# Performance work log

Measured on AMD Instinct MI355X. Metric: run time of the kernel, lower is better.

Reference implementation:

```python
import jax, jax.numpy as jnp
import numpy as np

N = 100000
E = 500000
MEM = 128
NODE = 128
TIME = 64
EDGE = 64
MEAN_DT = 0.0
STD_DT = 1.0
EPSILON = 0.1
GAMMA = 0.1
NUM_ITERS = 1


def setup_inputs() -> dict:
    key = jax.random.key(0)
    ks = jax.random.split(key, 20)

    def p(k, shape, fan_in):
        return jax.random.normal(k, shape, jnp.float32) * (1.0 / np.sqrt(fan_in))

    D_EDGE = EDGE + TIME  # TransformerConv edge_dim
    inp = {
        "x": jax.random.normal(ks[0], (N, MEM + NODE), jnp.float32),
        "last_update": jax.random.uniform(ks[1], (N,), jnp.float32) * 1000.0,
        "edge_index": jax.random.randint(ks[2], (2, E), 0, N),
        "t": jax.random.uniform(ks[3], (E,), jnp.float32) * 1000.0,
        "msg": jax.random.normal(ks[4], (E, EDGE), jnp.float32),
        # TimeEncoder: Linear(1, TIME) then cos
        "w_time": p(ks[5], (TIME,), 1),
        "b_time": jnp.zeros((TIME,), jnp.float32),
        # enc_x: Linear(MEM+NODE, MEM)
        "W_enc": p(ks[6], (MEM, MEM + NODE), MEM + NODE),
        "b_enc": jnp.zeros((MEM,), jnp.float32),
        # TransformerConv (heads=1, out=MEM, root_weight=False)
        "Wq": p(ks[7], (MEM, MEM), MEM),
        "bq": jnp.zeros((MEM,), jnp.float32),
        "Wk": p(ks[8], (MEM, MEM), MEM),
        "bk": jnp.zeros((MEM,), jnp.float32),
        "Wv": p(ks[9], (MEM, MEM), MEM),
        "bv": jnp.zeros((MEM,), jnp.float32),
        "We": p(ks[10], (MEM, D_EDGE), D_EDGE),  # lin_edge, bias=False
        # AntiSymmetricConv
        "W_anti": p(ks[11], (MEM, MEM), MEM),
        "b_anti": jnp.zeros((MEM,), jnp.float32),
    }
    return inp


def _forward(x, last_update, t, msg, w_time, b_time, W_enc, b_enc,
             Wq, bq, Wk, bk, Wv, bv, We, W_anti, b_anti, edge_index):
    src = edge_index[0]  # j (message source)
    dst = edge_index[1]  # i (aggregation target)

    # time encoding of relative times
    rel_t = jnp.abs(last_update[src] - t)
    rel_t = (rel_t - MEAN_DT) / STD_DT
    time_feat = jnp.cos(rel_t[:, None] * w_time[None, :] + b_time[None, :])  # [E, TIME]

    edge_attr = jnp.concatenate([msg, time_feat], axis=-1)  # [E, EDGE+TIME]
    e_proj = edge_attr @ We.T  # [E, MEM], lin_edge (no bias)

    h = x @ W_enc.T + b_enc  # [N, MEM]

    # antisymmetric weight
    A = W_anti - W_anti.T - GAMMA * jnp.eye(MEM, dtype=x.dtype)
    scale = 1.0 / np.sqrt(MEM)

    def phi(xc):
        # TransformerConv, heads=1, root_weight=False
        q = (xc @ Wq.T + bq)[dst]                 # [E, MEM]
        k = (xc @ Wk.T + bk)[src] + e_proj        # [E, MEM]
        v = (xc @ Wv.T + bv)[src] + e_proj        # [E, MEM]
        alpha = jnp.sum(q * k, axis=-1) * scale   # [E]
        # segment softmax over destination nodes
        amax = jax.ops.segment_max(alpha, dst, num_segments=N)
        amax = jnp.where(jnp.isfinite(amax), amax, 0.0)
        ex = jnp.exp(alpha - amax[dst])
        denom = jax.ops.segment_sum(ex, dst, num_segments=N) + 1e-16
        w = ex / denom[dst]
        return jax.ops.segment_sum(w[:, None] * v, dst, num_segments=N)  # [N, MEM]

    for _ in range(NUM_ITERS):
        g = phi(h)
        g = h @ A.T + g + b_anti
        g = jnp.tanh(g)
        h = h + EPSILON * g

    return jnp.tanh(h)


def reference(x, last_update, edge_index, t, msg, w_time, b_time, W_enc, b_enc,
              Wq, bq, Wk, bk, Wv, bv, We, W_anti, b_anti):
    return _forward(x, last_update, t, msg, w_time, b_time, W_enc, b_enc,
                    Wq, bq, Wk, bk, Wv, bv, We, W_anti, b_anti, edge_index)
```

## Files before the change

kernel.cpp:

```cpp
#include <hip/hip_runtime.h>
#include <hip/hip_bf16.h>
#include <math.h>

#define N_NODES 100000
#define N_EDGES 500000
#define MEM 128
#define IN_DIM 256
#define EDGEF 64
#define D_EDGE 128
#define EPSILON 0.1f
#define GAMMA 0.1f
#define SCALE 0.08838834764831845f

#define NPB 8
#define NT 32
#define XP 264
#define HP 136
#define ET 64
#define EA_LD 200

typedef __attribute__((ext_vector_type(8))) short bf16x8;
typedef __attribute__((ext_vector_type(4))) float f32x4;

__device__ __forceinline__ short f2bs(float f) {
    __hip_bfloat16 b = __float2bfloat16(f);
    return *(short*)&b;
}
__device__ __forceinline__ float bs2f(short s) {
    __hip_bfloat16 b = *(__hip_bfloat16*)&s;
    return __bfloat162float(b);
}
__device__ __forceinline__ float2 up2(unsigned int u) {
    float2 r;
    r.x = __uint_as_float(u << 16);
    r.y = __uint_as_float(u & 0xffff0000u);
    return r;
}
__device__ __forceinline__ unsigned int pk2(float lo, float hi) {
    return (unsigned int)(unsigned short)f2bs(lo)
         | ((unsigned int)(unsigned short)f2bs(hi) << 16);
}
__device__ __forceinline__ void atomic_pk_add_bf16(unsigned short* addr, unsigned int data) {
    asm volatile("global_atomic_pk_add_bf16 %0, %1, off"
                 :: "v"(addr), "v"(data) : "memory");
}

__global__ void k_prep(const float* __restrict__ W_anti, const float* __restrict__ We,
                       const float* __restrict__ W_enc,
                       const float* __restrict__ Wq, const float* __restrict__ Wk,
                       const float* __restrict__ Wv,
                       float* __restrict__ Abuf, unsigned short* __restrict__ Web,
                       unsigned short* __restrict__ WencH, unsigned short* __restrict__ WencL,
                       unsigned short* __restrict__ Wqb, unsigned short* __restrict__ Wkb,
                       unsigned short* __restrict__ Wvb) {
    int idx = blockIdx.x * blockDim.x + threadIdx.x;
    float w = W_enc[idx];
    short hi = f2bs(w);
    WencH[idx] = (unsigned short)hi;
    WencL[idx] = (unsigned short)f2bs(w - bs2f(hi));
    if (idx < 16384) {
        int m = idx >> 7, d = idx & 127;
        float a = W_anti[m * 128 + d] - W_anti[d * 128 + m];
        if (m == d) a -= GAMMA;
        Abuf[idx] = a;
        Web[idx] = (unsigned short)f2bs(We[idx]);
        Wqb[idx] = (unsigned short)f2bs(Wq[idx]);
        Wkb[idx] = (unsigned short)f2bs(Wk[idx]);
        Wvb[idx] = (unsigned short)f2bs(Wv[idx]);
    }
}

__global__ __launch_bounds__(256) void k_node_proj(
    const float* __restrict__ x,
    const float* __restrict__ b_enc, const float* __restrict__ bq,
    const float* __restrict__ bk, const float* __restrict__ bv,
    const unsigned short* __restrict__ WencH, const unsigned short* __restrict__ WencL,
    const unsigned short* __restrict__ Wqb, const unsigned short* __restrict__ Wkb,
    const unsigned short* __restrict__ Wvb,
    float* __restrict__ h, unsigned short* __restrict__ q,
    unsigned short* __restrict__ k, unsigned short* __restrict__ v)
{
    __shared__ short xhi[NT][XP];
    __shared__ short xlo[NT][XP];
    __shared__ short hb[NT][HP];
    const int tid = threadIdx.x;
    const int n0 = blockIdx.x * NT;

    {
        int r = tid >> 3, seg = tid & 7;
        const float4* xp = (const float4*)(x + (size_t)(n0 + r) * IN_DIM + seg * 32);
        unsigned int* dh = (unsigned int*)&xhi[r][seg * 32];
        unsigned int* dl = (unsigned int*)&xlo[r][seg * 32];
#pragma unroll
        for (int i = 0; i < 8; i++) {
            float4 a = xp[i];
            float fs[4] = {a.x, a.y, a.z, a.w};
            unsigned short h2[4], l2[4];
#pragma unroll
            for (int j = 0; j < 4; j++) {
                short hbit = f2bs(fs[j]);
                h2[j] = (unsigned short)hbit;
                l2[j] = (unsigned short)f2bs(fs[j] - bs2f(hbit));
            }
            dh[2 * i]     = h2[0] | ((unsigned int)h2[1] << 16);
            dh[2 * i + 1] = h2[2] | ((unsigned int)h2[3] << 16);
            dl[2 * i]     = l2[0] | ((unsigned int)l2[1] << 16);
            dl[2 * i + 1] = l2[2] | ((unsigned int)l2[3] << 16);
        }
    }
    __syncthreads();

    const int wave = tid >> 6, lane = tid & 63;
    const int quad = lane >> 4, l16 = lane & 15;
    const int mt = wave & 1;
    const int nh = wave >> 1;

    f32x4 acc[4];
#pragma unroll
    for (int i = 0; i < 4; i++) acc[i] = (f32x4){0.f, 0.f, 0.f, 0.f};
#pragma unroll
    for (int ko = 0; ko < 8; ko++) {
        bf16x8 ah = *(const bf16x8*)&xhi[mt * 16 + l16][ko * 32 + quad * 8];
        bf16x8 al = *(const bf16x8*)&xlo[mt * 16 + l16][ko * 32 + quad * 8];
#pragma unroll
        for (int i = 0; i < 4; i++) {
            size_t boff = (size_t)(nh * 64 + i * 16 + l16) * IN_DIM + ko * 32 + quad * 8;
            bf16x8 bh = *(const bf16x8*)(WencH + boff);
            bf16x8 bl = *(const bf16x8*)(WencL + boff);
            acc[i] = __builtin_amdgcn_mfma_f32_16x16x32_bf16(ah, bh, acc[i], 0, 0, 0);
            acc[i] = __builtin_amdgcn_mfma_f32_16x16x32_bf16(al, bh, acc[i], 0, 0, 0);
            acc[i] = __builtin_amdgcn_mfma_f32_16x16x32_bf16(ah, bl, acc[i], 0, 0, 0);
        }
    }
#pragma unroll
    for (int i = 0; i < 4; i++) {
        int col = nh * 64 + i * 16 + l16;
        float be = b_enc[col];
#pragma unroll
        for (int r = 0; r < 4; r++) {
            int row = mt * 16 + quad * 4 + r;
            float hv = acc[i][r] + be;
            h[(size_t)(n0 + row) * MEM + col] = hv;
            hb[row][col] = f2bs(hv);
        }
    }
    __syncthreads();

#define QKV(Wb, BIAS, OUT)                                                        \
    {                                                                             \
        f32x4 a2[4];                                                              \
        for (int i = 0; i < 4; i++) a2[i] = (f32x4){0.f, 0.f, 0.f, 0.f};          \
        for (int ko = 0; ko < 4; ko++) {                                          \
            bf16x8 a = *(const bf16x8*)&hb[mt * 16 + l16][ko * 32 + quad * 8];    \
            for (int i = 0; i < 4; i++) {                                         \
                size_t boff = (size_t)(nh * 64 + i * 16 + l16) * MEM              \
                            + ko * 32 + quad * 8;                                 \
                bf16x8 b = *(const bf16x8*)(Wb + boff);                           \
                a2[i] = __builtin_amdgcn_mfma_f32_16x16x32_bf16(a, b, a2[i], 0, 0, 0); \
            }                                                                     \
        }                                                                         \
        for (int i = 0; i < 4; i++) {                                             \
            int col = nh * 64 + i * 16 + l16;                                     \
            float bb = BIAS[col];                                                 \
            for (int r = 0; r < 4; r++) {                                         \
                int row = mt * 16 + quad * 4 + r;                                 \
                OUT[(size_t)(n0 + row) * MEM + col] =                             \
                    (unsigned short)f2bs(a2[i][r] + bb);                          \
            }                                                                     \
        }                                                                         \
    }
    QKV(Wqb, bq, q)
    QKV(Wkb, bk, k)
    QKV(Wvb, bv, v)
#undef QKV
}

__global__ __launch_bounds__(256, 6) void k_edge_all(
    const int* __restrict__ ei, const float* __restrict__ last_update,
    const float* __restrict__ t, const float* __restrict__ msg,
    const float* __restrict__ w_time, const float* __restrict__ b_time,
    const unsigned short* __restrict__ Web,
    const unsigned short* __restrict__ q, const unsigned short* __restrict__ k,
    const unsigned short* __restrict__ v,
    unsigned short* __restrict__ agg, float* __restrict__ denom)
{
    __shared__ short sE[ET][EA_LD];
    __shared__ int s_src[ET], s_dst[ET];
    __shared__ float s_rel[ET];

    const int tid = threadIdx.x;
    const size_t e0 = (size_t)blockIdx.x * ET;

    if (tid < ET) {
        size_t e = e0 + tid;
        if (e < N_EDGES) {
            int sn = ei[e];
            s_src[tid] = sn;
            s_dst[tid] = ei[N_EDGES + e];
            s_rel[tid] = fabsf(last_update[sn] - t[e]);
        } else {
            s_src[tid] = 0; s_dst[tid] = 0; s_rel[tid] = 0.f;
        }
    }
    __syncthreads();

    {
        int j = tid >> 2, seg = tid & 3, k0 = seg * 32;
        size_t e = e0 + j;
        bool valid = (e < N_EDGES);
        float vals[32];
        if (seg < 2) {
            if (valid) {
                const float4* mp = (const float4*)(msg + e * EDGEF + k0);
#pragma unroll
                for (int i = 0; i < 8; i++) {
                    float4 a = mp[i];
                    vals[4 * i] = a.x; vals[4 * i + 1] = a.y;
                    vals[4 * i + 2] = a.z; vals[4 * i + 3] = a.w;
                }
            } else {
#pragma unroll
                for (int i = 0; i < 32; i++) vals[i] = 0.f;
            }
        } else {
            int td = k0 - 64;
            float rel = s_rel[j];
            const float4* wtp = (const float4*)(w_time + td);
            const float4* btp = (const float4*)(b_time + td);
#pragma unroll
            for (int i = 0; i < 8; i++) {
                float4 wt = wtp[i];
                float4 bt = btp[i];
                vals[4 * i]     = valid ? __cosf(rel * wt.x + bt.x) : 0.f;
                vals[4 * i + 1] = valid ? __cosf(rel * wt.y + bt.y) : 0.f;
                vals[4 * i + 2] = valid ? __cosf(rel * wt.z + bt.z) : 0.f;
                vals[4 * i + 3] = valid ? __cosf(rel * wt.w + bt.w) : 0.f;
            }
        }
        unsigned int* dp = (unsigned int*)&sE[j][k0];
#pragma unroll
        for (int i = 0; i < 16; i++) {
            unsigned int lo = (unsigned short)f2bs(vals[2 * i]);
            unsigned int hi = (unsigned short)f2bs(vals[2 * i + 1]);
            dp[i] = lo | (hi << 16);
        }
    }
    __syncthreads();

    const int wave = tid >> 6, lane = tid & 63;
    const int quad = lane >> 4, l16 = lane & 15;

    f32x4 acc[8];
#pragma unroll
    for (int i = 0; i < 8; i++) acc[i] = (f32x4){0.f, 0.f, 0.f, 0.f};
#pragma unroll
    for (int ko = 0; ko < 4; ko++) {
        bf16x8 a = *(const bf16x8*)&sE[wave * 16 + l16][ko * 32 + quad * 8];
#pragma unroll
        for (int i = 0; i < 8; i++) {
            bf16x8 b = *(const bf16x8*)(Web + (size_t)(i * 16 + l16) * D_EDGE + ko * 32 + quad * 8);
            acc[i] = __builtin_amdgcn_mfma_f32_16x16x32_bf16(a, b, acc[i], 0, 0, 0);
        }
    }
    __syncthreads();
#pragma unroll
    for (int i = 0; i < 8; i++)
#pragma unroll
        for (int r = 0; r < 4; r++)
            sE[wave * 16 + quad * 4 + r][i * 16 + l16] = f2bs(acc[i][r]);
    __syncthreads();

    const int base = wave * 16;
    const int d2 = lane * 2;
    if (e0 + base < N_EDGES) {
        for (int jj = 0; jj < 16; jj += 2) {
            int ja = base + jj, jb = ja + 1;
            int sa = s_src[ja], da = s_dst[ja];
            int sb = s_src[jb], db = s_dst[jb];
            float2 epa = up2(*(const unsigned int*)&sE[ja][d2]);
            float2 epb = up2(*(const unsigned int*)&sE[jb][d2]);
            float2 qa = up2(*(const unsigned int*)(q + (size_t)da * MEM + d2));
            float2 qb2 = up2(*(const unsigned int*)(q + (size_t)db * MEM + d2));
            float2 ka = up2(*(const unsigned int*)(k + (size_t)sa * MEM + d2));
            float2 kb2 = up2(*(const unsigned int*)(k + (size_t)sb * MEM + d2));
            float pa = qa.x * (ka.x + epa.x) + qa.y * (ka.y + epa.y);
            float pb = qb2.x * (kb2.x + epb.x) + qb2.y * (kb2.y + epb.y);
#pragma unroll
            for (int off = 1; off < 64; off <<= 1) {
                pa += __shfl_xor(pa, off, 64);
                pb += __shfl_xor(pb, off, 64);
            }
            float exa = __expf(pa * SCALE);
            float exb = __expf(pb * SCALE);
            float2 va = up2(*(const unsigned int*)(v + (size_t)sa * MEM + d2));
            float2 vb = up2(*(const unsigned int*)(v + (size_t)sb * MEM + d2));
            unsigned int pka = pk2(exa * (va.x + epa.x), exa * (va.y + epa.y));
            unsigned int pkb = pk2(exb * (vb.x + epb.x), exb * (vb.y + epb.y));
            atomic_pk_add_bf16(agg + (size_t)da * MEM + d2, pka);
            atomic_pk_add_bf16(agg + (size_t)db * MEM + d2, pkb);
            if (lane == 0) {
                unsafeAtomicAdd(&denom[da], exa);
                unsafeAtomicAdd(&denom[db], exb);
            }
        }
    }
}

__global__ __launch_bounds__(128) void k_final(
    const float* __restrict__ h, const unsigned short* __restrict__ agg,
    const float* __restrict__ denom, const float* __restrict__ Abuf,
    const float* __restrict__ b_anti, float* __restrict__ out)
{
    __shared__ float hsh[NPB][MEM];
    const int m = threadIdx.x;
    const int n0 = blockIdx.x * NPB;
    for (int j = 0; j < NPB; j++) hsh[j][m] = h[(size_t)(n0 + j) * MEM + m];
    __syncthreads();
    float acc[NPB];
    float ba = b_anti[m];
    for (int j = 0; j < NPB; j++) {
        float dn = denom[n0 + j] + 1e-16f;
        float ag = bs2f((short)agg[(size_t)(n0 + j) * MEM + m]);
        acc[j] = ba + ag / dn;
    }
    const float4* A4 = (const float4*)(Abuf + (size_t)m * MEM);
    for (int d4 = 0; d4 < MEM / 4; d4++) {
        float4 w = A4[d4];
        int d = d4 * 4;
        for (int j = 0; j < NPB; j++)
            acc[j] += w.x * hsh[j][d] + w.y * hsh[j][d + 1] + w.z * hsh[j][d + 2] + w.w * hsh[j][d + 3];
    }
    for (int j = 0; j < NPB; j++) {
        float hv = hsh[j][m] + EPSILON * tanhf(acc[j]);
        out[(size_t)(n0 + j) * MEM + m] = tanhf(hv);
    }
}

extern "C" void kernel_launch(void* const* d_in, const int* in_sizes, int n_in,
                              void* d_out, int out_size, void* d_ws, size_t ws_size,
                              hipStream_t stream) {
    const float* x          = (const float*)d_in[0];
    const float* last_update= (const float*)d_in[1];
    const int*   ei         = (const int*)  d_in[2];
    const float* t          = (const float*)d_in[3];
    const float* msg        = (const float*)d_in[4];
    const float* w_time     = (const float*)d_in[5];
    const float* b_time     = (const float*)d_in[6];
    const float* W_enc      = (const float*)d_in[7];
    const float* b_enc      = (const float*)d_in[8];
    const float* Wq         = (const float*)d_in[9];
    const float* bq         = (const float*)d_in[10];
    const float* Wk         = (const float*)d_in[11];
    const float* bk         = (const float*)d_in[12];
    const float* Wv         = (const float*)d_in[13];
    const float* bv         = (const float*)d_in[14];
    const float* We         = (const float*)d_in[15];
    const float* W_anti     = (const float*)d_in[16];
    const float* b_anti     = (const float*)d_in[17];
    float* out = (float*)d_out;

    float* ws = (float*)d_ws;
    size_t nm = (size_t)N_NODES * MEM;
    float* h     = ws;
    float* Abuf  = h + nm;
    unsigned short* agg = (unsigned short*)(Abuf + MEM * MEM);
    float* denom = (float*)(agg + nm);
    unsigned short* qb    = (unsigned short*)(denom + N_NODES);
    unsigned short* kb    = qb + nm;
    unsigned short* vb    = kb + nm;
    unsigned short* Web   = vb + nm;
    unsigned short* WencH = Web + 16384;
    unsigned short* WencL = WencH + 32768;
    unsigned short* Wqb   = WencL + 32768;
    unsigned short* Wkb   = Wqb + 16384;
    unsigned short* Wvb   = Wkb + 16384;

    hipMemsetAsync(agg, 0, nm * sizeof(unsigned short) + N_NODES * sizeof(float), stream);
    k_prep<<<128, 256, 0, stream>>>(W_anti, We, W_enc, Wq, Wk, Wv,
                                    Abuf, Web, WencH, WencL, Wqb, Wkb, Wvb);

    k_node_proj<<<N_NODES / NT, 256, 0, stream>>>(
        x, b_enc, bq, bk, bv, WencH, WencL, Wqb, Wkb, Wvb, h, qb, kb, vb);

    k_edge_all<<<(N_EDGES + ET - 1) / ET, 256, 0, stream>>>(
        ei, last_update, t, msg, w_time, b_time, Web, qb, kb, vb, agg, denom);

    k_final<<<N_NODES / NPB, 128, 0, stream>>>(h, agg, denom, Abuf, b_anti, out);
}
```

Baseline: 806.5 us.

## Sort edges by destination and merge per-destination atomics in edge kernel

```diff
diff --git a/kernel.cpp b/kernel.cpp
--- a/kernel.cpp
+++ b/kernel.cpp
@@ -70,6 +70,63 @@
     }
 }
 
+
+__global__ void k_hist(const int* __restrict__ ei, int* __restrict__ cnt) {
+    int e = blockIdx.x * 256 + threadIdx.x;
+    if (e < N_EDGES) atomicAdd(&cnt[ei[N_EDGES + e]], 1);
+}
+
+__global__ __launch_bounds__(1024) void k_scan(const int* __restrict__ cnt,
+                                               int* __restrict__ cur) {
+    __shared__ int wsum[16];
+    __shared__ int btot;
+    const int tid = threadIdx.x;
+    const int lane = tid & 63, wid = tid >> 6;
+    int carry = 0;
+    for (int base = 0; base < N_NODES; base += 1024) {
+        int i = base + tid;
+        int x = (i < N_NODES) ? cnt[i] : 0;
+        int incl = x;
+#pragma unroll
+        for (int off = 1; off < 64; off <<= 1) {
+            int y = __shfl_up(incl, off, 64);
+            if (lane >= off) incl += y;
+        }
+        if (lane == 63) wsum[wid] = incl;
+        __syncthreads();
+        if (tid < 16) {
+            int w = wsum[tid];
+            int wincl = w;
+#pragma unroll
+            for (int off = 1; off < 16; off <<= 1) {
+                int y = __shfl_up(wincl, off, 64);
+                if (tid >= off) wincl += y;
+            }
+            wsum[tid] = wincl - w;
+            if (tid == 15) btot = wincl;
+        }
+        __syncthreads();
+        int excl = incl - x + wsum[wid] + carry;
+        if (i < N_NODES) cur[i] = excl;
+        carry += btot;
+    }
+}
+
+__global__ void k_scatter(const int* __restrict__ ei, const float* __restrict__ last_update,
+                          const float* __restrict__ t, int* __restrict__ cur,
+                          int* __restrict__ eid_s, int* __restrict__ src_s,
+                          int* __restrict__ dst_s, float* __restrict__ rel_s) {
+    int e = blockIdx.x * 256 + threadIdx.x;
+    if (e < N_EDGES) {
+        int dn = ei[N_EDGES + e], sn = ei[e];
+        int pos = atomicAdd(&cur[dn], 1);
+        eid_s[pos] = e;
+        src_s[pos] = sn;
+        dst_s[pos] = dn;
+        rel_s[pos] = fabsf(last_update[sn] - t[e]);
+    }
+}
+
 __global__ __launch_bounds__(256) void k_node_proj(
     const float* __restrict__ x,
     const float* __restrict__ b_enc, const float* __restrict__ bq,
@@ -176,8 +233,9 @@
 }
 
 __global__ __launch_bounds__(256, 6) void k_edge_all(
-    const int* __restrict__ ei, const float* __restrict__ last_update,
-    const float* __restrict__ t, const float* __restrict__ msg,
+    const int* __restrict__ eid_s, const int* __restrict__ src_s,
+    const int* __restrict__ dst_s, const float* __restrict__ rel_s,
+    const float* __restrict__ msg,
     const float* __restrict__ w_time, const float* __restrict__ b_time,
     const unsigned short* __restrict__ Web,
     const unsigned short* __restrict__ q, const unsigned short* __restrict__ k,
@@ -185,7 +243,7 @@
     unsigned short* __restrict__ agg, float* __restrict__ denom)
 {
     __shared__ short sE[ET][EA_LD];
-    __shared__ int s_src[ET], s_dst[ET];
+    __shared__ int s_src[ET], s_dst[ET], s_eid[ET];
     __shared__ float s_rel[ET];
 
     const int tid = threadIdx.x;
@@ -194,24 +252,23 @@
     if (tid < ET) {
         size_t e = e0 + tid;
         if (e < N_EDGES) {
-            int sn = ei[e];
-            s_src[tid] = sn;
-            s_dst[tid] = ei[N_EDGES + e];
-            s_rel[tid] = fabsf(last_update[sn] - t[e]);
+            s_eid[tid] = eid_s[e];
+            s_src[tid] = src_s[e];
+            s_dst[tid] = dst_s[e];
+            s_rel[tid] = rel_s[e];
         } else {
-            s_src[tid] = 0; s_dst[tid] = 0; s_rel[tid] = 0.f;
+            s_eid[tid] = 0; s_src[tid] = 0; s_dst[tid] = 0; s_rel[tid] = 0.f;
         }
     }
     __syncthreads();
 
     {
         int j = tid >> 2, seg = tid & 3, k0 = seg * 32;
-        size_t e = e0 + j;
-        bool valid = (e < N_EDGES);
+        bool valid = (e0 + j < N_EDGES);
         float vals[32];
         if (seg < 2) {
             if (valid) {
-                const float4* mp = (const float4*)(msg + e * EDGEF + k0);
+                const float4* mp = (const float4*)(msg + (size_t)s_eid[j] * EDGEF + k0);
 #pragma unroll
                 for (int i = 0; i < 8; i++) {
                     float4 a = mp[i];
@@ -273,14 +330,21 @@
     const int base = wave * 16;
     const int d2 = lane * 2;
     if (e0 + base < N_EDGES) {
+        int cur_dst = s_dst[base];
+        float2 qr = up2(*(const unsigned int*)(q + (size_t)cur_dst * MEM + d2));
+        float avx = 0.f, avy = 0.f, aex = 0.f;
         for (int jj = 0; jj < 16; jj += 2) {
             int ja = base + jj, jb = ja + 1;
             int sa = s_src[ja], da = s_dst[ja];
             int sb = s_src[jb], db = s_dst[jb];
+            float2 qa = qr;
+            if (da != cur_dst)
+                qa = up2(*(const unsigned int*)(q + (size_t)da * MEM + d2));
+            float2 qb2 = qa;
+            if (db != da)
+                qb2 = up2(*(const unsigned int*)(q + (size_t)db * MEM + d2));
             float2 epa = up2(*(const unsigned int*)&sE[ja][d2]);
             float2 epb = up2(*(const unsigned int*)&sE[jb][d2]);
-            float2 qa = up2(*(const unsigned int*)(q + (size_t)da * MEM + d2));
-            float2 qb2 = up2(*(const unsigned int*)(q + (size_t)db * MEM + d2));
             float2 ka = up2(*(const unsigned int*)(k + (size_t)sa * MEM + d2));
             float2 kb2 = up2(*(const unsigned int*)(k + (size_t)sb * MEM + d2));
             float pa = qa.x * (ka.x + epa.x) + qa.y * (ka.y + epa.y);
@@ -294,15 +358,22 @@
             float exb = __expf(pb * SCALE);
             float2 va = up2(*(const unsigned int*)(v + (size_t)sa * MEM + d2));
             float2 vb = up2(*(const unsigned int*)(v + (size_t)sb * MEM + d2));
-            unsigned int pka = pk2(exa * (va.x + epa.x), exa * (va.y + epa.y));
-            unsigned int pkb = pk2(exb * (vb.x + epb.x), exb * (vb.y + epb.y));
-            atomic_pk_add_bf16(agg + (size_t)da * MEM + d2, pka);
-            atomic_pk_add_bf16(agg + (size_t)db * MEM + d2, pkb);
-            if (lane == 0) {
-                unsafeAtomicAdd(&denom[da], exa);
-                unsafeAtomicAdd(&denom[db], exb);
-            }
-        }
+            if (da != cur_dst) {
+                atomic_pk_add_bf16(agg + (size_t)cur_dst * MEM + d2, pk2(avx, avy));
+                if (lane == 0) unsafeAtomicAdd(&denom[cur_dst], aex);
+                cur_dst = da; avx = 0.f; avy = 0.f; aex = 0.f;
+            }
+            avx += exa * (va.x + epa.x); avy += exa * (va.y + epa.y); aex += exa;
+            if (db != cur_dst) {
+                atomic_pk_add_bf16(agg + (size_t)cur_dst * MEM + d2, pk2(avx, avy));
+                if (lane == 0) unsafeAtomicAdd(&denom[cur_dst], aex);
+                cur_dst = db; avx = 0.f; avy = 0.f; aex = 0.f;
+            }
+            avx += exb * (vb.x + epb.x); avy += exb * (vb.y + epb.y); aex += exb;
+            qr = qb2;
+        }
+        atomic_pk_add_bf16(agg + (size_t)cur_dst * MEM + d2, pk2(avx, avy));
+        if (lane == 0) unsafeAtomicAdd(&denom[cur_dst], aex);
     }
 }
 
@@ -365,7 +436,13 @@
     float* Abuf  = h + nm;
     unsigned short* agg = (unsigned short*)(Abuf + MEM * MEM);
     float* denom = (float*)(agg + nm);
-    unsigned short* qb    = (unsigned short*)(denom + N_NODES);
+    int*   cnt   = (int*)(denom + N_NODES);
+    int*   cur   = cnt + N_NODES;
+    int*   eid_s = cur + N_NODES;
+    int*   src_s = eid_s + N_EDGES;
+    int*   dst_s = src_s + N_EDGES;
+    float* rel_s = (float*)(dst_s + N_EDGES);
+    unsigned short* qb    = (unsigned short*)(rel_s + N_EDGES);
     unsigned short* kb    = qb + nm;
     unsigned short* vb    = kb + nm;
     unsigned short* Web   = vb + nm;
@@ -375,15 +452,21 @@
     unsigned short* Wkb   = Wqb + 16384;
     unsigned short* Wvb   = Wkb + 16384;
 
-    hipMemsetAsync(agg, 0, nm * sizeof(unsigned short) + N_NODES * sizeof(float), stream);
+    hipMemsetAsync(agg, 0, nm * sizeof(unsigned short) + N_NODES * (sizeof(float) + sizeof(int)),
+                   stream);
     k_prep<<<128, 256, 0, stream>>>(W_anti, We, W_enc, Wq, Wk, Wv,
                                     Abuf, Web, WencH, WencL, Wqb, Wkb, Wvb);
 
+    k_hist<<<(N_EDGES + 255) / 256, 256, 0, stream>>>(ei, cnt);
+    k_scan<<<1, 1024, 0, stream>>>(cnt, cur);
+    k_scatter<<<(N_EDGES + 255) / 256, 256, 0, stream>>>(
+        ei, last_update, t, cur, eid_s, src_s, dst_s, rel_s);
+
     k_node_proj<<<N_NODES / NT, 256, 0, stream>>>(
         x, b_enc, bq, bk, bv, WencH, WencL, Wqb, Wkb, Wvb, h, qb, kb, vb);
 
     k_edge_all<<<(N_EDGES + ET - 1) / ET, 256, 0, stream>>>(
-        ei, last_update, t, msg, w_time, b_time, Web, qb, kb, vb, agg, denom);
+        eid_s, src_s, dst_s, rel_s, msg, w_time, b_time, Web, qb, kb, vb, agg, denom);
 
     k_final<<<N_NODES / NPB, 128, 0, stream>>>(h, agg, denom, Abuf, b_anti, out);
 }
```

New measurement: 935.1 us. 15.9% more time.
